# Optimization experiments

Measured on AMD Instinct MI355X. Metric: run time of the kernel, lower is better.

## Reference

```python
import math
import jax, jax.numpy as jnp
import numpy as np

D_MODEL = 1024
NUM_HEADS = 16
HEAD_DIM = D_MODEL // NUM_HEADS
THETA = 10000.0
BATCH = 4
SEQ = 2048


def apply_rope(x, token_positions, theta=THETA):
    # x: [b, h, s, d]; token_positions: [s] (broadcast over batch/heads)
    d = x.shape[-1]
    inv_freq = theta ** (-jnp.arange(0, d, 2, dtype=jnp.float32) / d)  # [d/2]
    angles = token_positions.astype(jnp.float32)[:, None] * inv_freq[None, :]  # [s, d/2]
    cos, sin = jnp.cos(angles), jnp.sin(angles)  # [s, d/2]
    x1 = x[..., 0::2]
    x2 = x[..., 1::2]
    out_even = x1 * cos - x2 * sin
    out_odd = x1 * sin + x2 * cos
    # interleave even/odd back: [..., s, d/2, 2] -> [..., s, d]
    return jnp.stack([out_even, out_odd], axis=-1).reshape(x.shape)


def setup_inputs() -> dict:
    key = jax.random.key(0)
    ks = jax.random.split(key, 5)
    std = math.sqrt(2.0 / D_MODEL)
    return {
        "in_features": jax.random.normal(ks[0], (BATCH, SEQ, D_MODEL), dtype=jnp.float32),
        "token_positions": jnp.arange(SEQ, dtype=jnp.int64 if jax.config.jax_enable_x64 else jnp.int32),
        "q_proj_weight": jax.random.normal(ks[1], (D_MODEL, D_MODEL), dtype=jnp.float32) * std,
        "k_proj_weight": jax.random.normal(ks[2], (D_MODEL, D_MODEL), dtype=jnp.float32) * std,
        "v_proj_weight": jax.random.normal(ks[3], (D_MODEL, D_MODEL), dtype=jnp.float32) * std,
        "out_proj_weight": jax.random.normal(ks[4], (D_MODEL, D_MODEL), dtype=jnp.float32) * std,
    }


def reference(in_features, token_positions, q_proj_weight, k_proj_weight, v_proj_weight, out_proj_weight):
    b, s, _ = in_features.shape
    h, hd = NUM_HEADS, HEAD_DIM

    def proj(w):
        # y = x @ w.T  -> [b, s, d_model] then split heads -> [b, h, s, hd]
        y = jnp.einsum('bsd,kd->bsk', in_features, w)
        return y.reshape(b, s, h, hd).transpose(0, 2, 1, 3)

    q = apply_rope(proj(q_proj_weight), token_positions)
    k = apply_rope(proj(k_proj_weight), token_positions)
    v = proj(v_proj_weight)

    scores = jnp.einsum('bhqd,bhkd->bhqk', q, k) / math.sqrt(hd)
    causal = jnp.tril(jnp.ones((s, s), dtype=bool))
    scores = jnp.where(causal, scores, jnp.float32(-1e9))
    attn = jax.nn.softmax(scores, axis=-1)
    out = jnp.einsum('bhqk,bhkd->bhqd', attn, v)  # [b, h, s, hd]
    merged = out.transpose(0, 2, 1, 3).reshape(b, s, h * hd)
    return jnp.einsum('bsv,dv->bsd', merged, out_proj_weight)
```

## Files before the change

kernel.cpp:

```cpp
#include <hip/hip_runtime.h>
#include <stdint.h>

#define D_MODEL 1024
#define NUM_HEADS 16
#define HEAD_DIM 64
#define BATCH 4
#define SEQ 2048
#define BS (BATCH*SEQ)
#define NX ((size_t)BS*D_MODEL)
#define WELEMS ((size_t)D_MODEL*D_MODEL)

typedef short bf16x8 __attribute__((ext_vector_type(8)));
typedef short bf16x4 __attribute__((ext_vector_type(4)));
typedef float f32x4  __attribute__((ext_vector_type(4)));

__device__ inline float b2f(short u) {
  unsigned x = ((unsigned)(unsigned short)u) << 16;
  union { unsigned u; float f; } c; c.u = x; return c.f;
}
__device__ inline short f2b(float f) {
  union { float f; unsigned u; } c; c.f = f;
  unsigned r = (c.u + 0x7FFFu + ((c.u >> 16) & 1u)) >> 16;
  return (short)r;
}
__device__ inline unsigned cvt_pk(float lo, float hi) {
  unsigned r;
  asm("v_cvt_pk_bf16_f32 %0, %1, %2" : "=v"(r) : "v"(lo), "v"(hi));
  return r;
}

typedef const __attribute__((address_space(1))) void* gas_t;
typedef __attribute__((address_space(3))) void*       las_t;
__device__ inline void gload16(const void* g, void* l) {
  __builtin_amdgcn_global_load_lds((gas_t)(uintptr_t)g,
                                   (las_t)(uint32_t)(uintptr_t)l, 16, 0, 0);
}

__global__ __launch_bounds__(256) void prep_convert(
    const float* __restrict__ X,
    const float* __restrict__ Wq, const float* __restrict__ Wk,
    const float* __restrict__ Wv, const float* __restrict__ Wo,
    short* __restrict__ Xb, short* __restrict__ Wb)
{
  size_t i = ((size_t)blockIdx.x * 256 + threadIdx.x) * 4;
  const float* src; short* dst; size_t off;
  if (i < NX) { src = X; dst = Xb; off = i; }
  else {
    size_t wi = i - NX;
    int w = (int)(wi >> 20);
    off = wi & (WELEMS - 1);
    src = (w == 0) ? Wq : (w == 1) ? Wk : (w == 2) ? Wv : Wo;
    dst = Wb + (size_t)w * WELEMS;
  }
  float4 v = *(const float4*)(src + off);
  bf16x4 o;
  o[0] = f2b(v.x); o[1] = f2b(v.y); o[2] = f2b(v.z); o[3] = f2b(v.w);
  *(bf16x4*)(dst + off) = o;
}

__global__ __launch_bounds__(256) void rope_table(
    const int* __restrict__ pos, float2* __restrict__ tab)
{
  int idx = blockIdx.x * 256 + threadIdx.x;
  int s = idx >> 5, i = idx & 31;
  float p = (float)pos[s];
  float inv = exp2f(-0.41524101186098287f * (float)i);
  float a = p * inv;
  tab[idx] = make_float2(cosf(a), sinf(a));
}

template<bool BF16OUT>
__global__ __launch_bounds__(256) void gemm_bt(
    const short* __restrict__ A, const short* __restrict__ Bw,
    void* __restrict__ outv, const int M, const int N, const int K,
    const size_t strideB, const size_t strideOut)
{
  __shared__ short Ash[128 * 32];
  __shared__ short Bsh[128 * 32];
  const int tid = threadIdx.x;
  const int wid = tid >> 6, lane = tid & 63;
  const int g = lane >> 4, li = lane & 15;
  const int row0 = blockIdx.y * 128, col0 = blockIdx.x * 128;
  const int wr = wid >> 1, wc = wid & 1;
  const short* Bz = Bw + (size_t)blockIdx.z * strideB;

  const short* Ag = A  + (size_t)(row0 + wid * 32 + (lane >> 2)) * K + (lane & 3) * 8;
  const short* Bg = Bz + (size_t)(col0 + wid * 32 + (lane >> 2)) * K + (lane & 3) * 8;
  short* lA = &Ash[wid * 1024];
  short* lB = &Bsh[wid * 1024];

  f32x4 acc[4][4];
#pragma unroll
  for (int i = 0; i < 4; ++i)
#pragma unroll
    for (int j = 0; j < 4; ++j) acc[i][j] = (f32x4){0.f, 0.f, 0.f, 0.f};

  for (int kt = 0; kt < K; kt += 32) {
    gload16(Ag + kt,                 lA);
    gload16(Ag + kt + (size_t)16*K,  lA + 512);
    gload16(Bg + kt,                 lB);
    gload16(Bg + kt + (size_t)16*K,  lB + 512);
    __syncthreads();
    bf16x8 af[4], bfv[4];
#pragma unroll
    for (int mm = 0; mm < 4; ++mm)
      af[mm] = *(const bf16x8*)&Ash[(wr * 64 + mm * 16 + li) * 32 + g * 8];
#pragma unroll
    for (int nn = 0; nn < 4; ++nn)
      bfv[nn] = *(const bf16x8*)&Bsh[(wc * 64 + nn * 16 + li) * 32 + g * 8];
#pragma unroll
    for (int mm = 0; mm < 4; ++mm)
#pragma unroll
      for (int nn = 0; nn < 4; ++nn)
        acc[mm][nn] = __builtin_amdgcn_mfma_f32_16x16x32_bf16(
            af[mm], bfv[nn], acc[mm][nn], 0, 0, 0);
    __syncthreads();
  }

  if (BF16OUT) {
    short* out = (short*)outv + (size_t)blockIdx.z * strideOut;
#pragma unroll
    for (int mm = 0; mm < 4; ++mm)
#pragma unroll
      for (int nn = 0; nn < 4; ++nn)
#pragma unroll
        for (int j = 0; j < 4; ++j) {
          int r = row0 + wr * 64 + mm * 16 + g * 4 + j;
          int c = col0 + wc * 64 + nn * 16 + li;
          out[(size_t)r * N + c] = f2b(acc[mm][nn][j]);
        }
  } else {
    float* out = (float*)outv;
#pragma unroll
    for (int mm = 0; mm < 4; ++mm)
#pragma unroll
      for (int nn = 0; nn < 4; ++nn)
#pragma unroll
        for (int j = 0; j < 4; ++j) {
          int r = row0 + wr * 64 + mm * 16 + g * 4 + j;
          int c = col0 + wc * 64 + nn * 16 + li;
          out[(size_t)r * N + c] = acc[mm][nn][j];
        }
  }
}

__global__ __launch_bounds__(256) void rope_apply(
    short* __restrict__ QK, const float2* __restrict__ tab)
{
  size_t idx = (size_t)blockIdx.x * 256 + threadIdx.x;
  short* base = QK + (size_t)blockIdx.y * NX + idx * 8;
  size_t e = idx * 8;
  int s  = (int)((e >> 10) & (SEQ - 1));
  int dd = (int)(e & (D_MODEL - 1));
  int i0 = (dd & 63) >> 1;
  const float2* tp = tab + s * 32 + i0;
  bf16x8 v = *(bf16x8*)base;
#pragma unroll
  for (int k = 0; k < 4; ++k) {
    float2 cs = tp[k];
    float ev = b2f(v[2 * k]), ov = b2f(v[2 * k + 1]);
    v[2 * k]     = f2b(ev * cs.x - ov * cs.y);
    v[2 * k + 1] = f2b(ev * cs.y + ov * cs.x);
  }
  *(bf16x8*)base = v;
}

__global__ __launch_bounds__(256) void transpose_v(
    const short* __restrict__ V, short* __restrict__ Vt)
{
  __shared__ short tile[64][72];
  const int s0 = blockIdx.x * 64, h = blockIdx.y, b = blockIdx.z;
  const int t = threadIdx.x;
  const short* src = V + ((size_t)(b * SEQ + s0)) * D_MODEL + h * 64;
#pragma unroll
  for (int it = 0; it < 2; ++it) {
    int r = it * 32 + (t >> 3), c0 = (t & 7) * 8;
    *(bf16x8*)&tile[r][c0] = *(const bf16x8*)(src + (size_t)r * D_MODEL + c0);
  }
  __syncthreads();
  short* dst = Vt + ((size_t)(b * NUM_HEADS + h) * 64) * SEQ + s0;
#pragma unroll
  for (int it = 0; it < 2; ++it) {
    int d = it * 32 + (t >> 3), sOff = (t & 7) * 8;
    bf16x8 v;
#pragma unroll
    for (int j = 0; j < 8; ++j) v[j] = tile[sOff + j][d];
    *(bf16x8*)(dst + (size_t)d * SEQ + sOff) = v;
  }
}

#define EXPSCALE 0.18033688011112043f
#define MASKV   -30000.0f

__global__ __launch_bounds__(256, 3) void flash_attn(
    const short* __restrict__ Q, const short* __restrict__ K,
    const short* __restrict__ Vt, short* __restrict__ O)
{
  __shared__ short Ksh[2][64 * 64];
  __shared__ short Vsh[2][64 * 64];
  __shared__ short Pl[4][32 * 64];
  const int qtb = (int)(gridDim.x - 1 - blockIdx.x);
  const int h = blockIdx.y, b = blockIdx.z;
  const int tid = threadIdx.x;
  const int wid = tid >> 6, lane = tid & 63;
  const int g = lane >> 4, li = lane & 15;
  const int qrow0 = qtb * 128 + wid * 32;
  const int tmaxBlk = 2 * qtb + 1;
  const int wtmax = (qrow0 + 31) >> 6;
  const size_t bS = (size_t)b * SEQ;

  const short* Qb = Q  + (bS + qrow0) * D_MODEL + h * 64;
  const short* Kb = K  + bS * D_MODEL + h * 64;
  const short* Vb = Vt + (size_t)(b * NUM_HEADS + h) * 64 * SEQ;
  short* Pw = &Pl[wid][0];

  const int sl  = lane;
  const int srr = sl >> 3;
  const int cs  = (sl & 7) ^ (srr & 7);
  const int rB  = wid * 8 + srr;

#define STAGE(buf, t) {                                                      \
    const size_t kr0 = (size_t)((t) * 64 + rB) * D_MODEL + cs * 8;           \
    const size_t kr1 = (size_t)((t) * 64 + rB + 32) * D_MODEL + cs * 8;      \
    gload16(Kb + kr0, &Ksh[buf][(wid * 8) * 64]);                            \
    gload16(Kb + kr1, &Ksh[buf][(32 + wid * 8) * 64]);                       \
    const size_t vr0 = (size_t)rB * SEQ + (t) * 64 + cs * 8;                 \
    const size_t vr1 = (size_t)(rB + 32) * SEQ + (t) * 64 + cs * 8;          \
    gload16(Vb + vr0, &Vsh[buf][(wid * 8) * 64]);                            \
    gload16(Vb + vr1, &Vsh[buf][(32 + wid * 8) * 64]);                       \
  }

  bf16x8 qb[2][2];
#pragma unroll
  for (int m = 0; m < 2; ++m)
#pragma unroll
    for (int hf = 0; hf < 2; ++hf)
      qb[m][hf] = *(const bf16x8*)(Qb + (size_t)(m * 16 + li) * D_MODEL
                                      + hf * 32 + g * 8);

  f32x4 oacc[2][4];
#pragma unroll
  for (int m = 0; m < 2; ++m)
#pragma unroll
    for (int n = 0; n < 4; ++n) oacc[m][n] = (f32x4){0.f, 0.f, 0.f, 0.f};
  float mrow[2] = {MASKV, MASKV};
  float lrow[2] = {0.f, 0.f};

  const int swz = (li & 7) << 3;

  STAGE(0, 0);
  __syncthreads();

  for (int t = 0; t <= tmaxBlk; ++t) {
    const int cur = t & 1;
    if (t < tmaxBlk) STAGE(cur ^ 1, t + 1);

    if (t <= wtmax) {
      const short* Kc = &Ksh[cur][0];
      const short* Vc = &Vsh[cur][0];
      f32x4 sc[2][4];
      __builtin_amdgcn_s_setprio(1);
#pragma unroll
      for (int n = 0; n < 4; ++n) {
        bf16x8 kb0 = *(const bf16x8*)&Kc[(n * 16 + li) * 64 + (((0 * 4 + g) ^ (li & 7)) << 3)];
        bf16x8 kb1 = *(const bf16x8*)&Kc[(n * 16 + li) * 64 + (((1 * 4 + g) ^ (li & 7)) << 3)];
#pragma unroll
        for (int m = 0; m < 2; ++m) {
          f32x4 a = (f32x4){0.f, 0.f, 0.f, 0.f};
          a = __builtin_amdgcn_mfma_f32_16x16x32_bf16(kb0, qb[m][0], a, 0, 0, 0);
          a = __builtin_amdgcn_mfma_f32_16x16x32_bf16(kb1, qb[m][1], a, 0, 0, 0);
          sc[m][n] = a;
        }
      }
      __builtin_amdgcn_s_setprio(0);
      if (t == wtmax) {
#pragma unroll
        for (int m = 0; m < 2; ++m) {
          int qg = qrow0 + m * 16 + li;
#pragma unroll
          for (int n = 0; n < 4; ++n)
#pragma unroll
            for (int j = 0; j < 4; ++j) {
              int kg = t * 64 + n * 16 + g * 4 + j;
              if (kg > qg) sc[m][n][j] = MASKV;
            }
        }
      }
#pragma unroll
      for (int m = 0; m < 2; ++m) {
        float a0 = fmaxf(fmaxf(sc[m][0][0], sc[m][0][1]), fmaxf(sc[m][0][2], sc[m][0][3]));
        float a1 = fmaxf(fmaxf(sc[m][1][0], sc[m][1][1]), fmaxf(sc[m][1][2], sc[m][1][3]));
        float a2 = fmaxf(fmaxf(sc[m][2][0], sc[m][2][1]), fmaxf(sc[m][2][2], sc[m][2][3]));
        float a3 = fmaxf(fmaxf(sc[m][3][0], sc[m][3][1]), fmaxf(sc[m][3][2], sc[m][3][3]));
        float pm = fmaxf(fmaxf(a0, a1), fmaxf(a2, a3));
        pm = fmaxf(pm, __shfl_xor(pm, 16, 64));
        pm = fmaxf(pm, __shfl_xor(pm, 32, 64));
        if (!__all(pm <= mrow[m] + 16.6f)) {
          float mn = fmaxf(mrow[m], pm);
          float corr = exp2f((mrow[m] - mn) * EXPSCALE);
          mrow[m] = mn;
          lrow[m] *= corr;
#pragma unroll
          for (int n = 0; n < 4; ++n)
#pragma unroll
            for (int j = 0; j < 4; ++j) oacc[m][n][j] *= corr;
        }
        float mnS = mrow[m] * EXPSCALE;
        float rs = 0.f;
#pragma unroll
        for (int n = 0; n < 4; ++n) {
#pragma unroll
          for (int j = 0; j < 4; ++j) {
            float p = exp2f(__builtin_fmaf(sc[m][n][j], EXPSCALE, -mnS));
            sc[m][n][j] = p;
            rs += p;
          }
        }
        rs += __shfl_xor(rs, 16, 64);
        rs += __shfl_xor(rs, 32, 64);
        lrow[m] += rs;
#pragma unroll
        for (int n = 0; n < 4; ++n) {
          uint2 w2;
          w2.x = cvt_pk(sc[m][n][0], sc[m][n][1]);
          w2.y = cvt_pk(sc[m][n][2], sc[m][n][3]);
          *(uint2*)&Pw[(m * 16 + li) * 64 + ((n * 16 + g * 4) ^ swz)] = w2;
        }
      }
      __builtin_amdgcn_s_setprio(1);
#pragma unroll
      for (int n = 0; n < 4; ++n) {
        bf16x8 vb0 = *(const bf16x8*)&Vc[(n * 16 + li) * 64 + (((0 * 4 + g) ^ (li & 7)) << 3)];
        bf16x8 vb1 = *(const bf16x8*)&Vc[(n * 16 + li) * 64 + (((1 * 4 + g) ^ (li & 7)) << 3)];
#pragma unroll
        for (int m = 0; m < 2; ++m) {
          bf16x8 pb0 = *(const bf16x8*)&Pw[(m * 16 + li) * 64 + (((0 * 4 + g) ^ (li & 7)) << 3)];
          bf16x8 pb1 = *(const bf16x8*)&Pw[(m * 16 + li) * 64 + (((1 * 4 + g) ^ (li & 7)) << 3)];
          oacc[m][n] = __builtin_amdgcn_mfma_f32_16x16x32_bf16(vb0, pb0, oacc[m][n], 0, 0, 0);
          oacc[m][n] = __builtin_amdgcn_mfma_f32_16x16x32_bf16(vb1, pb1, oacc[m][n], 0, 0, 0);
        }
      }
      __builtin_amdgcn_s_setprio(0);
    }
    __syncthreads();
  }

#pragma unroll
  for (int m = 0; m < 2; ++m) {
    float linv = 1.f / lrow[m];
#pragma unroll
    for (int n = 0; n < 4; ++n) {
      uint2 w2;
      w2.x = cvt_pk(oacc[m][n][0] * linv, oacc[m][n][1] * linv);
      w2.y = cvt_pk(oacc[m][n][2] * linv, oacc[m][n][3] * linv);
      *(uint2*)(O + (bS + qrow0 + m * 16 + li) * D_MODEL
                  + h * 64 + n * 16 + g * 4) = w2;
    }
  }
#undef STAGE
}

extern "C" void kernel_launch(void* const* d_in, const int* in_sizes, int n_in,
                              void* d_out, int out_size, void* d_ws, size_t ws_size,
                              hipStream_t stream) {
  const float* X  = (const float*)d_in[0];
  const int* pos  = (const int*)d_in[1];
  const float* Wq = (const float*)d_in[2];
  const float* Wk = (const float*)d_in[3];
  const float* Wv = (const float*)d_in[4];
  const float* Wo = (const float*)d_in[5];

  char* ws = (char*)d_ws;
  short*  Xb  = (short*)(ws);
  short*  Wb  = (short*)(ws + 16777216);
  short*  QKV = (short*)(ws + 25165824);
  short*  Vt  = (short*)(ws + 75497472);
  short*  Ob  = (short*)(ws + 92274688);
  float2* tab = (float2*)(ws + 109051904);

  prep_convert<<<12288, 256, 0, stream>>>(X, Wq, Wk, Wv, Wo, Xb, Wb);
  rope_table<<<256, 256, 0, stream>>>(pos, tab);
  gemm_bt<true><<<dim3(8, 64, 3), 256, 0, stream>>>(
      Xb, Wb, QKV, BS, D_MODEL, D_MODEL, WELEMS, NX);
  rope_apply<<<dim3(4096, 2, 1), 256, 0, stream>>>(QKV, tab);
  transpose_v<<<dim3(32, 16, 4), 256, 0, stream>>>(QKV + 2 * NX, Vt);
  flash_attn<<<dim3(16, 16, 4), 256, 0, stream>>>(QKV, QKV + NX, Vt, Ob);
  gemm_bt<false><<<dim3(8, 64, 1), 256, 0, stream>>>(
      Ob, Wb + 3 * WELEMS, d_out, BS, D_MODEL, D_MODEL, 0, 0);
}
```

Before: 359.8 us.

## Triple-buffer K/V tiles in flash attention with vmcnt-based single barrier

Changes the flash attention K/V staging from double to triple buffering, prefetching two tiles ahead. Each iteration waits with a partial vmcnt and one raw s_barrier, replacing the two __syncthreads per tile. Launch bounds drop from 3 to 2 blocks per SM to make room for the larger LDS footprint. The aim is to hide global-load latency better, at the cost of occupancy. On the last iterations a dummy load of tile 0 is issued so the vmcnt arithmetic stays uniform.

```diff
diff --git a/kernel.cpp b/kernel.cpp
--- a/kernel.cpp
+++ b/kernel.cpp
@@ -192,12 +192,12 @@
 #define EXPSCALE 0.18033688011112043f
 #define MASKV   -30000.0f
 
-__global__ __launch_bounds__(256, 3) void flash_attn(
+__global__ __launch_bounds__(256, 2) void flash_attn(
     const short* __restrict__ Q, const short* __restrict__ K,
     const short* __restrict__ Vt, short* __restrict__ O)
 {
-  __shared__ short Ksh[2][64 * 64];
-  __shared__ short Vsh[2][64 * 64];
+  __shared__ short Ksh[3][64 * 64];
+  __shared__ short Vsh[3][64 * 64];
   __shared__ short Pl[4][32 * 64];
   const int qtb = (int)(gridDim.x - 1 - blockIdx.x);
   const int h = blockIdx.y, b = blockIdx.z;
@@ -214,9 +214,8 @@
   const short* Vb = Vt + (size_t)(b * NUM_HEADS + h) * 64 * SEQ;
   short* Pw = &Pl[wid][0];
 
-  const int sl  = lane;
-  const int srr = sl >> 3;
-  const int cs  = (sl & 7) ^ (srr & 7);
+  const int srr = lane >> 3;
+  const int cs  = (lane & 7) ^ (srr & 7);
   const int rB  = wid * 8 + srr;
 
 #define STAGE(buf, t) {                                                      \
@@ -237,6 +236,7 @@
     for (int hf = 0; hf < 2; ++hf)
       qb[m][hf] = *(const bf16x8*)(Qb + (size_t)(m * 16 + li) * D_MODEL
                                       + hf * 32 + g * 8);
+  asm volatile("s_waitcnt vmcnt(0)" ::: "memory");
 
   f32x4 oacc[2][4];
 #pragma unroll
@@ -246,14 +246,19 @@
   float mrow[2] = {MASKV, MASKV};
   float lrow[2] = {0.f, 0.f};
 
-  const int swz = (li & 7) << 3;
-
   STAGE(0, 0);
-  __syncthreads();
+  STAGE(1, 1);
 
   for (int t = 0; t <= tmaxBlk; ++t) {
-    const int cur = t & 1;
-    if (t < tmaxBlk) STAGE(cur ^ 1, t + 1);
+    const int cur = t % 3;
+    asm volatile("s_waitcnt vmcnt(4)" ::: "memory");
+    __builtin_amdgcn_s_barrier();
+    __builtin_amdgcn_sched_barrier(0);
+    {
+      const int ts = (t + 2 <= tmaxBlk) ? (t + 2) : 0;
+      const int bs3 = (t + 2) % 3;
+      STAGE(bs3, ts);
+    }
 
     if (t <= wtmax) {
       const short* Kc = &Ksh[cur][0];
@@ -262,8 +267,8 @@
       __builtin_amdgcn_s_setprio(1);
 #pragma unroll
       for (int n = 0; n < 4; ++n) {
-        bf16x8 kb0 = *(const bf16x8*)&Kc[(n * 16 + li) * 64 + (((0 * 4 + g) ^ (li & 7)) << 3)];
-        bf16x8 kb1 = *(const bf16x8*)&Kc[(n * 16 + li) * 64 + (((1 * 4 + g) ^ (li & 7)) << 3)];
+        bf16x8 kb0 = *(const bf16x8*)&Kc[(n * 16 + li) * 64 + ((g ^ (li & 7)) << 3)];
+        bf16x8 kb1 = *(const bf16x8*)&Kc[(n * 16 + li) * 64 + (((4 + g) ^ (li & 7)) << 3)];
 #pragma unroll
         for (int m = 0; m < 2; ++m) {
           f32x4 a = (f32x4){0.f, 0.f, 0.f, 0.f};
@@ -324,25 +329,24 @@
           uint2 w2;
           w2.x = cvt_pk(sc[m][n][0], sc[m][n][1]);
           w2.y = cvt_pk(sc[m][n][2], sc[m][n][3]);
-          *(uint2*)&Pw[(m * 16 + li) * 64 + ((n * 16 + g * 4) ^ swz)] = w2;
+          *(uint2*)&Pw[(m * 16 + li) * 64 + ((n * 16 + g * 4) ^ ((li & 7) << 3))] = w2;
         }
       }
       __builtin_amdgcn_s_setprio(1);
 #pragma unroll
       for (int n = 0; n < 4; ++n) {
-        bf16x8 vb0 = *(const bf16x8*)&Vc[(n * 16 + li) * 64 + (((0 * 4 + g) ^ (li & 7)) << 3)];
-        bf16x8 vb1 = *(const bf16x8*)&Vc[(n * 16 + li) * 64 + (((1 * 4 + g) ^ (li & 7)) << 3)];
+        bf16x8 vb0 = *(const bf16x8*)&Vc[(n * 16 + li) * 64 + ((g ^ (li & 7)) << 3)];
+        bf16x8 vb1 = *(const bf16x8*)&Vc[(n * 16 + li) * 64 + (((4 + g) ^ (li & 7)) << 3)];
 #pragma unroll
         for (int m = 0; m < 2; ++m) {
-          bf16x8 pb0 = *(const bf16x8*)&Pw[(m * 16 + li) * 64 + (((0 * 4 + g) ^ (li & 7)) << 3)];
-          bf16x8 pb1 = *(const bf16x8*)&Pw[(m * 16 + li) * 64 + (((1 * 4 + g) ^ (li & 7)) << 3)];
+          bf16x8 pb0 = *(const bf16x8*)&Pw[(m * 16 + li) * 64 + ((g ^ (li & 7)) << 3)];
+          bf16x8 pb1 = *(const bf16x8*)&Pw[(m * 16 + li) * 64 + (((4 + g) ^ (li & 7)) << 3)];
           oacc[m][n] = __builtin_amdgcn_mfma_f32_16x16x32_bf16(vb0, pb0, oacc[m][n], 0, 0, 0);
           oacc[m][n] = __builtin_amdgcn_mfma_f32_16x16x32_bf16(vb1, pb1, oacc[m][n], 0, 0, 0);
         }
       }
       __builtin_amdgcn_s_setprio(0);
     }
-    __syncthreads();
   }
 
 #pragma unroll
```

After: 370.5 us. 3.0% more time.

## Switch flash attention to 32x32 MFMA with register-resident P via permlane swap

Applied to the files above, without the earlier changes.

Rewrites the attention inner loop to use 32x32x16 bf16 MFMAs and computes S transposed, so each lane owns a single query row. The P matrix is converted to bf16 and rearranged in registers with v_permlane32_swap instead of going through shared memory, which removes the P LDS round trip and the 16-lane shuffles. Diagonal tiles skip the fully masked 32-key half, and launch bounds go up to 4 blocks per CU. This adds register pressure from the 16-wide accumulators, and the grid size is now hardcoded as 16 query blocks.

```diff
diff --git a/kernel.cpp b/kernel.cpp
--- a/kernel.cpp
+++ b/kernel.cpp
@@ -13,6 +13,7 @@
 typedef short bf16x8 __attribute__((ext_vector_type(8)));
 typedef short bf16x4 __attribute__((ext_vector_type(4)));
 typedef float f32x4  __attribute__((ext_vector_type(4)));
+typedef float f32x16 __attribute__((ext_vector_type(16)));
 
 __device__ inline float b2f(short u) {
   unsigned x = ((unsigned)(unsigned short)u) << 16;
@@ -27,6 +28,9 @@
   unsigned r;
   asm("v_cvt_pk_bf16_f32 %0, %1, %2" : "=v"(r) : "v"(lo), "v"(hi));
   return r;
+}
+__device__ inline void pl32swap(unsigned &a, unsigned &b) {
+  asm("v_permlane32_swap_b32 %0, %1" : "+v"(a), "+v"(b));
 }
 
 typedef const __attribute__((address_space(1))) void* gas_t;
@@ -192,31 +196,27 @@
 #define EXPSCALE 0.18033688011112043f
 #define MASKV   -30000.0f
 
-__global__ __launch_bounds__(256, 3) void flash_attn(
+__global__ __launch_bounds__(256, 4) void flash_attn(
     const short* __restrict__ Q, const short* __restrict__ K,
     const short* __restrict__ Vt, short* __restrict__ O)
 {
   __shared__ short Ksh[2][64 * 64];
   __shared__ short Vsh[2][64 * 64];
-  __shared__ short Pl[4][32 * 64];
-  const int qtb = (int)(gridDim.x - 1 - blockIdx.x);
+  const int qtb = 15 - (int)blockIdx.x;
   const int h = blockIdx.y, b = blockIdx.z;
   const int tid = threadIdx.x;
   const int wid = tid >> 6, lane = tid & 63;
-  const int g = lane >> 4, li = lane & 15;
+  const int q5 = lane & 31, hi = lane >> 5;
   const int qrow0 = qtb * 128 + wid * 32;
   const int tmaxBlk = 2 * qtb + 1;
   const int wtmax = (qrow0 + 31) >> 6;
   const size_t bS = (size_t)b * SEQ;
 
-  const short* Qb = Q  + (bS + qrow0) * D_MODEL + h * 64;
   const short* Kb = K  + bS * D_MODEL + h * 64;
   const short* Vb = Vt + (size_t)(b * NUM_HEADS + h) * 64 * SEQ;
-  short* Pw = &Pl[wid][0];
-
-  const int sl  = lane;
-  const int srr = sl >> 3;
-  const int cs  = (sl & 7) ^ (srr & 7);
+
+  const int srr = lane >> 3;
+  const int cs  = (lane & 7) ^ srr;
   const int rB  = wid * 8 + srr;
 
 #define STAGE(buf, t) {                                                      \
@@ -230,23 +230,17 @@
     gload16(Vb + vr1, &Vsh[buf][(32 + wid * 8) * 64]);                       \
   }
 
-  bf16x8 qb[2][2];
-#pragma unroll
-  for (int m = 0; m < 2; ++m)
-#pragma unroll
-    for (int hf = 0; hf < 2; ++hf)
-      qb[m][hf] = *(const bf16x8*)(Qb + (size_t)(m * 16 + li) * D_MODEL
-                                      + hf * 32 + g * 8);
-
-  f32x4 oacc[2][4];
-#pragma unroll
-  for (int m = 0; m < 2; ++m)
-#pragma unroll
-    for (int n = 0; n < 4; ++n) oacc[m][n] = (f32x4){0.f, 0.f, 0.f, 0.f};
-  float mrow[2] = {MASKV, MASKV};
-  float lrow[2] = {0.f, 0.f};
-
-  const int swz = (li & 7) << 3;
+  bf16x8 qb[4];
+  {
+    const short* Qp = Q + (bS + qrow0 + q5) * D_MODEL + h * 64 + hi * 8;
+#pragma unroll
+    for (int d = 0; d < 4; ++d) qb[d] = *(const bf16x8*)(Qp + d * 16);
+  }
+
+  f32x16 acc0, acc1;
+#pragma unroll
+  for (int r = 0; r < 16; ++r) { acc0[r] = 0.f; acc1[r] = 0.f; }
+  float mrow = MASKV, lrow = 0.f;
 
   STAGE(0, 0);
   __syncthreads();
@@ -258,103 +252,135 @@
     if (t <= wtmax) {
       const short* Kc = &Ksh[cur][0];
       const short* Vc = &Vsh[cur][0];
-      f32x4 sc[2][4];
+      const bool diag = (t == wtmax);
+      const bool full = !diag || (wid & 1);
+
+      f32x16 sc0, sc1;
+#pragma unroll
+      for (int r = 0; r < 16; ++r) { sc0[r] = 0.f; sc1[r] = 0.f; }
       __builtin_amdgcn_s_setprio(1);
 #pragma unroll
-      for (int n = 0; n < 4; ++n) {
-        bf16x8 kb0 = *(const bf16x8*)&Kc[(n * 16 + li) * 64 + (((0 * 4 + g) ^ (li & 7)) << 3)];
-        bf16x8 kb1 = *(const bf16x8*)&Kc[(n * 16 + li) * 64 + (((1 * 4 + g) ^ (li & 7)) << 3)];
-#pragma unroll
-        for (int m = 0; m < 2; ++m) {
-          f32x4 a = (f32x4){0.f, 0.f, 0.f, 0.f};
-          a = __builtin_amdgcn_mfma_f32_16x16x32_bf16(kb0, qb[m][0], a, 0, 0, 0);
-          a = __builtin_amdgcn_mfma_f32_16x16x32_bf16(kb1, qb[m][1], a, 0, 0, 0);
-          sc[m][n] = a;
+      for (int d = 0; d < 4; ++d) {
+        bf16x8 ak = *(const bf16x8*)&Kc[q5 * 64 + (((2 * d + hi) ^ (q5 & 7)) << 3)];
+        sc0 = __builtin_amdgcn_mfma_f32_32x32x16_bf16(ak, qb[d], sc0, 0, 0, 0);
+      }
+      if (full) {
+#pragma unroll
+        for (int d = 0; d < 4; ++d) {
+          bf16x8 ak = *(const bf16x8*)&Kc[(32 + q5) * 64 + (((2 * d + hi) ^ (q5 & 7)) << 3)];
+          sc1 = __builtin_amdgcn_mfma_f32_32x32x16_bf16(ak, qb[d], sc1, 0, 0, 0);
         }
       }
       __builtin_amdgcn_s_setprio(0);
-      if (t == wtmax) {
-#pragma unroll
-        for (int m = 0; m < 2; ++m) {
-          int qg = qrow0 + m * 16 + li;
-#pragma unroll
-          for (int n = 0; n < 4; ++n)
-#pragma unroll
-            for (int j = 0; j < 4; ++j) {
-              int kg = t * 64 + n * 16 + g * 4 + j;
-              if (kg > qg) sc[m][n][j] = MASKV;
-            }
-        }
-      }
-#pragma unroll
-      for (int m = 0; m < 2; ++m) {
-        float a0 = fmaxf(fmaxf(sc[m][0][0], sc[m][0][1]), fmaxf(sc[m][0][2], sc[m][0][3]));
-        float a1 = fmaxf(fmaxf(sc[m][1][0], sc[m][1][1]), fmaxf(sc[m][1][2], sc[m][1][3]));
-        float a2 = fmaxf(fmaxf(sc[m][2][0], sc[m][2][1]), fmaxf(sc[m][2][2], sc[m][2][3]));
-        float a3 = fmaxf(fmaxf(sc[m][3][0], sc[m][3][1]), fmaxf(sc[m][3][2], sc[m][3][3]));
-        float pm = fmaxf(fmaxf(a0, a1), fmaxf(a2, a3));
-        pm = fmaxf(pm, __shfl_xor(pm, 16, 64));
+
+      if (diag) {
+#pragma unroll
+        for (int r = 0; r < 16; ++r) {
+          int off = (r & 3) + 8 * (r >> 2) + 4 * hi;
+          if (full) { if (off > q5) sc1[r] = MASKV; }
+          else      { if (off > q5) sc0[r] = MASKV; }
+        }
+      }
+
+      {
+        float t8[8];
+#pragma unroll
+        for (int r = 0; r < 8; ++r) t8[r] = fmaxf(sc0[2 * r], sc0[2 * r + 1]);
+        if (full) {
+#pragma unroll
+          for (int r = 0; r < 8; ++r)
+            t8[r] = fmaxf(t8[r], fmaxf(sc1[2 * r], sc1[2 * r + 1]));
+        }
+        float t4a = fmaxf(t8[0], t8[1]), t4b = fmaxf(t8[2], t8[3]);
+        float t4c = fmaxf(t8[4], t8[5]), t4d = fmaxf(t8[6], t8[7]);
+        float pm = fmaxf(fmaxf(t4a, t4b), fmaxf(t4c, t4d));
         pm = fmaxf(pm, __shfl_xor(pm, 32, 64));
-        if (!__all(pm <= mrow[m] + 16.6f)) {
-          float mn = fmaxf(mrow[m], pm);
-          float corr = exp2f((mrow[m] - mn) * EXPSCALE);
-          mrow[m] = mn;
-          lrow[m] *= corr;
-#pragma unroll
-          for (int n = 0; n < 4; ++n)
-#pragma unroll
-            for (int j = 0; j < 4; ++j) oacc[m][n][j] *= corr;
-        }
-        float mnS = mrow[m] * EXPSCALE;
-        float rs = 0.f;
-#pragma unroll
-        for (int n = 0; n < 4; ++n) {
-#pragma unroll
-          for (int j = 0; j < 4; ++j) {
-            float p = exp2f(__builtin_fmaf(sc[m][n][j], EXPSCALE, -mnS));
-            sc[m][n][j] = p;
-            rs += p;
-          }
-        }
-        rs += __shfl_xor(rs, 16, 64);
+        if (!__all(pm <= mrow + 16.6f)) {
+          float mn = fmaxf(mrow, pm);
+          float corr = exp2f((mrow - mn) * EXPSCALE);
+          mrow = mn;
+          lrow *= corr;
+#pragma unroll
+          for (int r = 0; r < 16; ++r) { acc0[r] *= corr; acc1[r] *= corr; }
+        }
+        float mnS = mrow * EXPSCALE;
+        float s8[8];
+#pragma unroll
+        for (int r = 0; r < 16; ++r)
+          sc0[r] = exp2f(__builtin_fmaf(sc0[r], EXPSCALE, -mnS));
+        if (full) {
+#pragma unroll
+          for (int r = 0; r < 16; ++r)
+            sc1[r] = exp2f(__builtin_fmaf(sc1[r], EXPSCALE, -mnS));
+#pragma unroll
+          for (int r = 0; r < 8; ++r)
+            s8[r] = (sc0[2 * r] + sc0[2 * r + 1]) + (sc1[2 * r] + sc1[2 * r + 1]);
+        } else {
+#pragma unroll
+          for (int r = 0; r < 8; ++r) s8[r] = sc0[2 * r] + sc0[2 * r + 1];
+        }
+        float u4a = s8[0] + s8[1], u4b = s8[2] + s8[3];
+        float u4c = s8[4] + s8[5], u4d = s8[6] + s8[7];
+        float rs = (u4a + u4b) + (u4c + u4d);
         rs += __shfl_xor(rs, 32, 64);
-        lrow[m] += rs;
-#pragma unroll
-        for (int n = 0; n < 4; ++n) {
-          uint2 w2;
-          w2.x = cvt_pk(sc[m][n][0], sc[m][n][1]);
-          w2.y = cvt_pk(sc[m][n][2], sc[m][n][3]);
-          *(uint2*)&Pw[(m * 16 + li) * 64 + ((n * 16 + g * 4) ^ swz)] = w2;
-        }
-      }
+        lrow += rs;
+      }
+
+      union U8 { unsigned u[4]; bf16x8 v; };
+      bf16x8 pb[4];
+      {
+        unsigned w[4][2];
+#pragma unroll
+        for (int s = 0; s < 4; ++s) {
+          w[s][0] = cvt_pk(sc0[4 * s + 0], sc0[4 * s + 1]);
+          w[s][1] = cvt_pk(sc0[4 * s + 2], sc0[4 * s + 3]);
+        }
+        pl32swap(w[0][0], w[1][0]); pl32swap(w[0][1], w[1][1]);
+        pl32swap(w[2][0], w[3][0]); pl32swap(w[2][1], w[3][1]);
+        U8 u0; u0.u[0] = w[0][0]; u0.u[1] = w[0][1]; u0.u[2] = w[1][0]; u0.u[3] = w[1][1];
+        U8 u1; u1.u[0] = w[2][0]; u1.u[1] = w[2][1]; u1.u[2] = w[3][0]; u1.u[3] = w[3][1];
+        pb[0] = u0.v; pb[1] = u1.v;
+      }
+      if (full) {
+        unsigned w[4][2];
+#pragma unroll
+        for (int s = 0; s < 4; ++s) {
+          w[s][0] = cvt_pk(sc1[4 * s + 0], sc1[4 * s + 1]);
+          w[s][1] = cvt_pk(sc1[4 * s + 2], sc1[4 * s + 3]);
+        }
+        pl32swap(w[0][0], w[1][0]); pl32swap(w[0][1], w[1][1]);
+        pl32swap(w[2][0], w[3][0]); pl32swap(w[2][1], w[3][1]);
+        U8 u0; u0.u[0] = w[0][0]; u0.u[1] = w[0][1]; u0.u[2] = w[1][0]; u0.u[3] = w[1][1];
+        U8 u1; u1.u[0] = w[2][0]; u1.u[1] = w[2][1]; u1.u[2] = w[3][0]; u1.u[3] = w[3][1];
+        pb[2] = u0.v; pb[3] = u1.v;
+      }
+
+      const int nkb = full ? 4 : 2;
       __builtin_amdgcn_s_setprio(1);
-#pragma unroll
-      for (int n = 0; n < 4; ++n) {
-        bf16x8 vb0 = *(const bf16x8*)&Vc[(n * 16 + li) * 64 + (((0 * 4 + g) ^ (li & 7)) << 3)];
-        bf16x8 vb1 = *(const bf16x8*)&Vc[(n * 16 + li) * 64 + (((1 * 4 + g) ^ (li & 7)) << 3)];
-#pragma unroll
-        for (int m = 0; m < 2; ++m) {
-          bf16x8 pb0 = *(const bf16x8*)&Pw[(m * 16 + li) * 64 + (((0 * 4 + g) ^ (li & 7)) << 3)];
-          bf16x8 pb1 = *(const bf16x8*)&Pw[(m * 16 + li) * 64 + (((1 * 4 + g) ^ (li & 7)) << 3)];
-          oacc[m][n] = __builtin_amdgcn_mfma_f32_16x16x32_bf16(vb0, pb0, oacc[m][n], 0, 0, 0);
-          oacc[m][n] = __builtin_amdgcn_mfma_f32_16x16x32_bf16(vb1, pb1, oacc[m][n], 0, 0, 0);
-        }
+      for (int kb = 0; kb < nkb; ++kb) {
+        bf16x8 av0 = *(const bf16x8*)&Vc[q5 * 64 + (((2 * kb + hi) ^ (q5 & 7)) << 3)];
+        acc0 = __builtin_amdgcn_mfma_f32_32x32x16_bf16(av0, pb[kb], acc0, 0, 0, 0);
+        bf16x8 av1 = *(const bf16x8*)&Vc[(32 + q5) * 64 + (((2 * kb + hi) ^ (q5 & 7)) << 3)];
+        acc1 = __builtin_amdgcn_mfma_f32_32x32x16_bf16(av1, pb[kb], acc1, 0, 0, 0);
       }
       __builtin_amdgcn_s_setprio(0);
     }
     __syncthreads();
   }
 
-#pragma unroll
-  for (int m = 0; m < 2; ++m) {
-    float linv = 1.f / lrow[m];
-#pragma unroll
-    for (int n = 0; n < 4; ++n) {
+  {
+    float linv = 1.f / lrow;
+    short* Op = O + (bS + qrow0 + q5) * D_MODEL + h * 64 + 4 * hi;
+#pragma unroll
+    for (int s = 0; s < 4; ++s) {
       uint2 w2;
-      w2.x = cvt_pk(oacc[m][n][0] * linv, oacc[m][n][1] * linv);
-      w2.y = cvt_pk(oacc[m][n][2] * linv, oacc[m][n][3] * linv);
-      *(uint2*)(O + (bS + qrow0 + m * 16 + li) * D_MODEL
-                  + h * 64 + n * 16 + g * 4) = w2;
+      w2.x = cvt_pk(acc0[4 * s + 0] * linv, acc0[4 * s + 1] * linv);
+      w2.y = cvt_pk(acc0[4 * s + 2] * linv, acc0[4 * s + 3] * linv);
+      *(uint2*)(Op + 8 * s) = w2;
+      uint2 w3;
+      w3.x = cvt_pk(acc1[4 * s + 0] * linv, acc1[4 * s + 1] * linv);
+      w3.y = cvt_pk(acc1[4 * s + 2] * linv, acc1[4 * s + 3] * linv);
+      *(uint2*)(Op + 32 + 8 * s) = w3;
     }
   }
 #undef STAGE
```

New measurement: 1.017 ms. 183% more time.
